# Kernel optimization log

Hardware: AMD Instinct MI355X
Metric: run time of the kernel (lower is better)

## Reference

```python
import jax, jax.numpy as jnp
import numpy as np
from jax.scipy.special import logsumexp

# Module hyperparameters
N_PARTS = 128
BATCH = 1024
# Entropic-regularized solver settings (differentiable surrogate for the
# cvxpylayers LP solve; eps small relative to O(1) eta-phi distances)
EPS = 0.02
ITERS = 100
LOG_FLOOR = 1e-30  # avoid log(0) for zero-mass dummy particles


def setup_inputs() -> dict:
    key = jax.random.key(0)
    k1, k2 = jax.random.split(key)
    # [B, n_parts, 3]: features (eta, phi, pt); uniform fill keeps pt > 0
    jets1 = jax.random.uniform(k1, (BATCH, N_PARTS, 3), dtype=jnp.float32)
    jets2 = jax.random.uniform(k2, (BATCH, N_PARTS, 3), dtype=jnp.float32)
    return {"jets1": jets1, "jets2": jets2}


def _sinkhorn_flow(C, loga, logb):
    """Batched log-domain Sinkhorn. C: [B,N,M], loga: [B,N], logb: [B,M].
    Returns the transport plan (flow) [B,N,M] with marginals ~ (a, b)."""
    f = jnp.zeros_like(loga)
    g = jnp.zeros_like(logb)

    def step(carry, _):
        f, g = carry
        f = EPS * (loga - logsumexp((g[:, None, :] - C) / EPS, axis=2))
        g = EPS * (logb - logsumexp((f[:, :, None] - C) / EPS, axis=1))
        return (f, g), None

    (f, g), _ = jax.lax.scan(step, (f, g), None, length=ITERS)
    return jnp.exp((f[:, :, None] + g[:, None, :] - C) / EPS)


def reference(jets1, jets2):
    n = jets1.shape[1]
    # Pairwise eta-phi ground distances: [B, n, n]
    diffs = -(jets1[:, :, None, :2] - jets2[:, None, :, :2]) + 1e-12
    dists = jnp.linalg.norm(diffs, axis=3)
    # pt weights (LP marginals)
    w1 = jets1[:, :, 2]
    w2 = jets2[:, :, 2]
    E1 = jnp.sum(w1, axis=1)
    E2 = jnp.sum(w2, axis=1)
    EabsDiff = jnp.abs(E2 - E1)
    # Partial OT (total mass = min(E1,E2), row/col sums <= w) is made balanced
    # by adding one zero-cost dummy particle per side absorbing the excess mass.
    a = jnp.concatenate([w1, jnp.maximum(E2 - E1, 0.0)[:, None]], axis=1)  # [B, n+1]
    b = jnp.concatenate([w2, jnp.maximum(E1 - E2, 0.0)[:, None]], axis=1)  # [B, n+1]
    Cp = jnp.pad(dists, ((0, 0), (0, 1), (0, 1)))  # dummy row/col have zero cost
    loga = jnp.log(jnp.maximum(a, LOG_FLOOR))
    logb = jnp.log(jnp.maximum(b, LOG_FLOOR))
    flow = _sinkhorn_flow(Cp, loga, logb)  # [B, n+1, n+1]
    # EMD = transport cost over real particles + energy-difference penalty
    emds = jnp.sum(dists * flow[:, :n, :n], axis=(1, 2)) + EabsDiff  # [B]
    return emds
```

## Files before the change

### kernel.cpp

```cpp
#include <hip/hip_runtime.h>

#define NP    128
#define NITER 100
#define RSC   72.13475204444817f
#define IRSC  0.013862943611198906f

typedef __attribute__((ext_vector_type(8))) short bf16x8;
typedef __attribute__((ext_vector_type(4))) float f32x4;

__device__ __forceinline__ float wsum64(float x) {
  #pragma unroll
  for (int s = 1; s < 64; s <<= 1) x += __shfl_xor(x, s);
  return x;
}
__device__ __forceinline__ float bf2f(unsigned short h) {
  return __uint_as_float(((unsigned)h) << 16);
}
__device__ __forceinline__ unsigned short f2bf(float f) {
  unsigned u = __float_as_uint(f);
  u += 0x7fffu + ((u >> 16) & 1u);
  return (unsigned short)(u >> 16);
}

__global__ __launch_bounds__(64, 1) void emd_sinkhorn(
    const float* __restrict__ j1g, const float* __restrict__ j2g,
    float* __restrict__ out)
{
  __shared__ __align__(16) float x1s[NP], y1s[NP], x2s[NP], y2s[NP];
  __shared__ __align__(16) float ahs[NP], bhs[NP];
  __shared__ __align__(16) float Slds[NP];
  __shared__ __align__(16) unsigned short Plds[NP];
  __shared__ __align__(16) unsigned short Qlds[NP];

  const int l  = threadIdx.x;
  const int lg = l >> 4;
  const int li = l & 15;
  const int b  = blockIdx.x;
  const float* J1 = j1g + (size_t)b * (NP * 3);
  const float* J2 = j2g + (size_t)b * (NP * 3);

  #pragma unroll
  for (int k = l; k < NP; k += 64) {
    x1s[k] = J1[3*k]; y1s[k] = J1[3*k+1]; ahs[k] = J1[3*k+2];
    x2s[k] = J2[3*k]; y2s[k] = J2[3*k+1]; bhs[k] = J2[3*k+2];
  }
  __syncthreads();

  const float e1 = wsum64(ahs[l] + ahs[l + 64]);
  const float e2 = wsum64(bhs[l] + bhs[l + 64]);
  const float dE = fabsf(e2 - e1);
  const float aslk = fmaxf(fmaxf(e2 - e1, 0.0f), 1e-30f);
  const float bslk = fmaxf(fmaxf(e1 - e2, 0.0f), 1e-30f);
  const float2 araw = *(const float2*)&ahs[2*l];
  const float2 braw = *(const float2*)&bhs[2*l];
  const float ah0 = fmaxf(araw.x, 1e-30f), ah1 = fmaxf(araw.y, 1e-30f);
  const float bh0 = fmaxf(braw.x, 1e-30f), bh1 = fmaxf(braw.y, 1e-30f);

  bf16x8 KA[8][4], KB[8][4];
  #pragma unroll
  for (int rt = 0; rt < 8; ++rt) {
    const float xr = x1s[16*rt + li], yr = y1s[16*rt + li];
    #pragma unroll
    for (int kt = 0; kt < 4; ++kt) {
      #pragma unroll
      for (int i2 = 0; i2 < 8; ++i2) {
        const int k = 32*kt + 8*lg + i2;
        const float dx = x2s[k] - xr + 1e-12f;
        const float dy = y2s[k] - yr + 1e-12f;
        KA[rt][kt][i2] = (short)f2bf(
            __builtin_amdgcn_exp2f(-__builtin_sqrtf(dx*dx + dy*dy) * RSC));
      }
    }
  }
  #pragma unroll
  for (int ct = 0; ct < 8; ++ct) {
    const float xc = x2s[16*ct + li], yc = y2s[16*ct + li];
    #pragma unroll
    for (int kt = 0; kt < 4; ++kt) {
      #pragma unroll
      for (int i2 = 0; i2 < 8; ++i2) {
        const int k = 32*kt + 8*lg + i2;
        const float dx = xc - x1s[k] + 1e-12f;
        const float dy = yc - y1s[k] + 1e-12f;
        KB[ct][kt][i2] = (short)f2bf(
            __builtin_amdgcn_exp2f(-__builtin_sqrtf(dx*dx + dy*dy) * RSC));
      }
    }
  }

  ((unsigned*)Qlds)[l] = 0x3F803F80u;
  float SQ = 128.0f, q128 = 1.0f;
  __syncthreads();

  for (int it = 0; it < NITER; ++it) {
    const float p128 = aslk * __builtin_amdgcn_rcpf(SQ + q128);

    bf16x8 qf[4];
    #pragma unroll
    for (int kt = 0; kt < 4; ++kt)
      qf[kt] = *(const bf16x8*)((const char*)Qlds + 64*kt + 16*lg);
    f32x4 acc[8];
    #pragma unroll
    for (int rt = 0; rt < 8; ++rt) {
      acc[rt] = (f32x4){q128, q128, q128, q128};
      #pragma unroll
      for (int kt = 0; kt < 4; ++kt)
        acc[rt] = __builtin_amdgcn_mfma_f32_16x16x32_bf16(
            KA[rt][kt], qf[kt], acc[rt], 0, 0, 0);
    }
    if (li == 0) {
      #pragma unroll
      for (int rt = 0; rt < 8; ++rt)
        *(f32x4*)&Slds[16*rt + 4*lg] = acc[rt];
    }
    __syncthreads();
    const float2 s2 = *(const float2*)&Slds[2*l];
    const float P0 = ah0 * __builtin_amdgcn_rcpf(s2.x);
    const float P1 = ah1 * __builtin_amdgcn_rcpf(s2.y);
    const float SP = wsum64(P0 + P1);
    const float q128n = bslk * __builtin_amdgcn_rcpf(SP + p128);
    ((unsigned*)Plds)[l] =
        (unsigned)f2bf(P0) | ((unsigned)f2bf(P1) << 16);
    __syncthreads();

    bf16x8 pf[4];
    #pragma unroll
    for (int kt = 0; kt < 4; ++kt)
      pf[kt] = *(const bf16x8*)((const char*)Plds + 64*kt + 16*lg);
    f32x4 acc2[8];
    #pragma unroll
    for (int ct = 0; ct < 8; ++ct) {
      acc2[ct] = (f32x4){p128, p128, p128, p128};
      #pragma unroll
      for (int kt = 0; kt < 4; ++kt)
        acc2[ct] = __builtin_amdgcn_mfma_f32_16x16x32_bf16(
            pf[kt], KB[ct][kt], acc2[ct], 0, 0, 0);
    }
    if (lg == 0) {
      #pragma unroll
      for (int ct = 0; ct < 8; ++ct)
        Slds[16*ct + li] = acc2[ct][0];
    }
    __syncthreads();
    const float2 t2 = *(const float2*)&Slds[2*l];
    const float Q0 = bh0 * __builtin_amdgcn_rcpf(t2.x);
    const float Q1 = bh1 * __builtin_amdgcn_rcpf(t2.y);
    SQ = wsum64(Q0 + Q1);
    ((unsigned*)Qlds)[l] =
        (unsigned)f2bf(Q0) | ((unsigned)f2bf(Q1) << 16);
    q128 = q128n;
    __syncthreads();
  }

  bf16x8 qf[4];
  #pragma unroll
  for (int kt = 0; kt < 4; ++kt)
    qf[kt] = *(const bf16x8*)((const char*)Qlds + 64*kt + 16*lg);
  float accE = 0.0f;
  #pragma unroll
  for (int rt = 0; rt < 8; ++rt) {
    const float Pn = bf2f(Plds[16*rt + li]);
    #pragma unroll
    for (int kt = 0; kt < 4; ++kt) {
      #pragma unroll
      for (int i2 = 0; i2 < 8; ++i2) {
        const float kk = bf2f((unsigned short)KA[rt][kt][i2]);
        const float qm = bf2f((unsigned short)qf[kt][i2]);
        const float d  = -__builtin_amdgcn_logf(kk) * IRSC;
        accE = fmaf(d, (Pn * kk) * qm, accE);
      }
    }
  }
  accE = wsum64(accE);
  if (l == 0) out[b] = accE + dE;
}

extern "C" void kernel_launch(void* const* d_in, const int* in_sizes, int n_in,
                              void* d_out, int out_size, void* d_ws, size_t ws_size,
                              hipStream_t stream) {
  const float* j1 = (const float*)d_in[0];
  const float* j2 = (const float*)d_in[1];
  float* outp = (float*)d_out;
  const int batch = in_sizes[0] / (NP * 3);
  hipLaunchKernelGGL(emd_sinkhorn, dim3(batch), dim3(64), 0, stream,
                     j1, j2, outp);
}
```

Measured before the change: 236.7 us.

## Split Sinkhorn matvecs across two waves and broadcast vectors via ds_bpermute

The block grows from one wave to two. Each wave holds half of the kernel matrices (4 row or column tiles instead of 8) and computes half of each matvec. Both waves redundantly compute the full P/Q vectors, and the MFMA operands are gathered from registers with ds_bpermute instead of LDS round trips. This drops two barriers per iteration, halves per-wave MFMA work and register footprint, and raises parallelism per batch element, at the cost of block-wide barriers between waves and duplicated scaling work.

Result: no change. 232.9 us (-1.6%).

```diff
diff --git a/kernel.cpp b/kernel.cpp
--- a/kernel.cpp
+++ b/kernel.cpp
@@ -22,27 +22,28 @@
   return (unsigned short)(u >> 16);
 }
 
-__global__ __launch_bounds__(64, 1) void emd_sinkhorn(
+__global__ __launch_bounds__(128, 2) void emd_sinkhorn(
     const float* __restrict__ j1g, const float* __restrict__ j2g,
     float* __restrict__ out)
 {
   __shared__ __align__(16) float x1s[NP], y1s[NP], x2s[NP], y2s[NP];
   __shared__ __align__(16) float ahs[NP], bhs[NP];
   __shared__ __align__(16) float Slds[NP];
-  __shared__ __align__(16) unsigned short Plds[NP];
-  __shared__ __align__(16) unsigned short Qlds[NP];
-
-  const int l  = threadIdx.x;
+  __shared__ __align__(16) float Tlds[NP];
+  __shared__ float red[2];
+
+  const int t  = threadIdx.x;
+  const int l  = t & 63;
+  const int wv = t >> 6;
   const int lg = l >> 4;
   const int li = l & 15;
   const int b  = blockIdx.x;
   const float* J1 = j1g + (size_t)b * (NP * 3);
   const float* J2 = j2g + (size_t)b * (NP * 3);
 
-  #pragma unroll
-  for (int k = l; k < NP; k += 64) {
-    x1s[k] = J1[3*k]; y1s[k] = J1[3*k+1]; ahs[k] = J1[3*k+2];
-    x2s[k] = J2[3*k]; y2s[k] = J2[3*k+1]; bhs[k] = J2[3*k+2];
+  if (t < NP) {
+    x1s[t] = J1[3*t]; y1s[t] = J1[3*t+1]; ahs[t] = J1[3*t+2];
+    x2s[t] = J2[3*t]; y2s[t] = J2[3*t+1]; bhs[t] = J2[3*t+2];
   }
   __syncthreads();
 
@@ -56,10 +57,11 @@
   const float ah0 = fmaxf(araw.x, 1e-30f), ah1 = fmaxf(araw.y, 1e-30f);
   const float bh0 = fmaxf(braw.x, 1e-30f), bh1 = fmaxf(braw.y, 1e-30f);
 
-  bf16x8 KA[8][4], KB[8][4];
-  #pragma unroll
-  for (int rt = 0; rt < 8; ++rt) {
-    const float xr = x1s[16*rt + li], yr = y1s[16*rt + li];
+  bf16x8 KA[4][4], KB[4][4];
+  #pragma unroll
+  for (int rt = 0; rt < 4; ++rt) {
+    const int n = 64*wv + 16*rt + li;
+    const float xr = x1s[n], yr = y1s[n];
     #pragma unroll
     for (int kt = 0; kt < 4; ++kt) {
       #pragma unroll
@@ -73,8 +75,9 @@
     }
   }
   #pragma unroll
-  for (int ct = 0; ct < 8; ++ct) {
-    const float xc = x2s[16*ct + li], yc = y2s[16*ct + li];
+  for (int ct = 0; ct < 4; ++ct) {
+    const int m = 64*wv + 16*ct + li;
+    const float xc = x2s[m], yc = y2s[m];
     #pragma unroll
     for (int kt = 0; kt < 4; ++kt) {
       #pragma unroll
@@ -88,20 +91,27 @@
     }
   }
 
-  ((unsigned*)Qlds)[l] = 0x3F803F80u;
+  unsigned Qpk = 0x3F803F80u;
+  unsigned Ppk = 0;
   float SQ = 128.0f, q128 = 1.0f;
-  __syncthreads();
 
   for (int it = 0; it < NITER; ++it) {
     const float p128 = aslk * __builtin_amdgcn_rcpf(SQ + q128);
 
     bf16x8 qf[4];
     #pragma unroll
-    for (int kt = 0; kt < 4; ++kt)
-      qf[kt] = *(const bf16x8*)((const char*)Qlds + 64*kt + 16*lg);
-    f32x4 acc[8];
-    #pragma unroll
-    for (int rt = 0; rt < 8; ++rt) {
+    for (int kt = 0; kt < 4; ++kt) {
+      union { unsigned u[4]; bf16x8 v; } r;
+      #pragma unroll
+      for (int q = 0; q < 4; ++q)
+        r.u[q] = (unsigned)__builtin_amdgcn_ds_bpermute(
+            4*(16*kt + 4*lg + q), (int)Qpk);
+      qf[kt] = r.v;
+    }
+
+    f32x4 acc[4];
+    #pragma unroll
+    for (int rt = 0; rt < 4; ++rt) {
       acc[rt] = (f32x4){q128, q128, q128, q128};
       #pragma unroll
       for (int kt = 0; kt < 4; ++kt)
@@ -110,26 +120,32 @@
     }
     if (li == 0) {
       #pragma unroll
-      for (int rt = 0; rt < 8; ++rt)
-        *(f32x4*)&Slds[16*rt + 4*lg] = acc[rt];
+      for (int rt = 0; rt < 4; ++rt)
+        *(f32x4*)&Slds[64*wv + 16*rt + 4*lg] = acc[rt];
     }
     __syncthreads();
+
     const float2 s2 = *(const float2*)&Slds[2*l];
     const float P0 = ah0 * __builtin_amdgcn_rcpf(s2.x);
     const float P1 = ah1 * __builtin_amdgcn_rcpf(s2.y);
     const float SP = wsum64(P0 + P1);
     const float q128n = bslk * __builtin_amdgcn_rcpf(SP + p128);
-    ((unsigned*)Plds)[l] =
-        (unsigned)f2bf(P0) | ((unsigned)f2bf(P1) << 16);
-    __syncthreads();
+    Ppk = (unsigned)f2bf(P0) | ((unsigned)f2bf(P1) << 16);
 
     bf16x8 pf[4];
     #pragma unroll
-    for (int kt = 0; kt < 4; ++kt)
-      pf[kt] = *(const bf16x8*)((const char*)Plds + 64*kt + 16*lg);
-    f32x4 acc2[8];
-    #pragma unroll
-    for (int ct = 0; ct < 8; ++ct) {
+    for (int kt = 0; kt < 4; ++kt) {
+      union { unsigned u[4]; bf16x8 v; } r;
+      #pragma unroll
+      for (int q = 0; q < 4; ++q)
+        r.u[q] = (unsigned)__builtin_amdgcn_ds_bpermute(
+            4*(16*kt + 4*lg + q), (int)Ppk);
+      pf[kt] = r.v;
+    }
+
+    f32x4 acc2[4];
+    #pragma unroll
+    for (int ct = 0; ct < 4; ++ct) {
       acc2[ct] = (f32x4){p128, p128, p128, p128};
       #pragma unroll
       for (int kt = 0; kt < 4; ++kt)
@@ -138,28 +154,36 @@
     }
     if (lg == 0) {
       #pragma unroll
-      for (int ct = 0; ct < 8; ++ct)
-        Slds[16*ct + li] = acc2[ct][0];
+      for (int ct = 0; ct < 4; ++ct)
+        Tlds[64*wv + 16*ct + li] = acc2[ct][0];
     }
     __syncthreads();
-    const float2 t2 = *(const float2*)&Slds[2*l];
+
+    const float2 t2 = *(const float2*)&Tlds[2*l];
     const float Q0 = bh0 * __builtin_amdgcn_rcpf(t2.x);
     const float Q1 = bh1 * __builtin_amdgcn_rcpf(t2.y);
     SQ = wsum64(Q0 + Q1);
-    ((unsigned*)Qlds)[l] =
-        (unsigned)f2bf(Q0) | ((unsigned)f2bf(Q1) << 16);
+    Qpk = (unsigned)f2bf(Q0) | ((unsigned)f2bf(Q1) << 16);
     q128 = q128n;
-    __syncthreads();
   }
 
   bf16x8 qf[4];
   #pragma unroll
-  for (int kt = 0; kt < 4; ++kt)
-    qf[kt] = *(const bf16x8*)((const char*)Qlds + 64*kt + 16*lg);
+  for (int kt = 0; kt < 4; ++kt) {
+    union { unsigned u[4]; bf16x8 v; } r;
+    #pragma unroll
+    for (int q = 0; q < 4; ++q)
+      r.u[q] = (unsigned)__builtin_amdgcn_ds_bpermute(
+          4*(16*kt + 4*lg + q), (int)Qpk);
+    qf[kt] = r.v;
+  }
   float accE = 0.0f;
   #pragma unroll
-  for (int rt = 0; rt < 8; ++rt) {
-    const float Pn = bf2f(Plds[16*rt + li]);
+  for (int rt = 0; rt < 4; ++rt) {
+    const int n = 64*wv + 16*rt + li;
+    const unsigned pr = (unsigned)__builtin_amdgcn_ds_bpermute(
+        4*(n >> 1), (int)Ppk);
+    const float Pn = bf2f((unsigned short)((li & 1) ? (pr >> 16) : pr));
     #pragma unroll
     for (int kt = 0; kt < 4; ++kt) {
       #pragma unroll
@@ -172,7 +196,9 @@
     }
   }
   accE = wsum64(accE);
-  if (l == 0) out[b] = accE + dE;
+  if (l == 0) red[wv] = accE;
+  __syncthreads();
+  if (t == 0) out[b] = (red[0] + red[1]) + dE;
 }
 
 extern "C" void kernel_launch(void* const* d_in, const int* in_sizes, int n_in,
@@ -182,6 +208,6 @@
   const float* j2 = (const float*)d_in[1];
   float* outp = (float*)d_out;
   const int batch = in_sizes[0] / (NP * 3);
-  hipLaunchKernelGGL(emd_sinkhorn, dim3(batch), dim3(64), 0, stream,
+  hipLaunchKernelGGL(emd_sinkhorn, dim3(batch), dim3(128), 0, stream,
                      j1, j2, outp);
 }
```

## Split each Sinkhorn problem across four wavefronts and drop redundant barriers

Applied to the files above, without the earlier changes.

Each block now uses 256 threads (four waves) instead of one wave. Each wave keeps a 32-row slice of the kernel matrices, so register use per wave drops and the serial MFMA chain per iteration is four times shorter. Every wave recomputes the full P and Q vectors and writes identical values to shared memory, which lets two of the four barriers per iteration go; a separate T buffer keeps the two matrix-vector phases from clobbering each other. The cost is redundant normalization work in every wave and a small cross-wave reduction at the end.

New measurement: 201.6 us. 1.17x faster.

```diff
diff --git a/kernel.cpp b/kernel.cpp
--- a/kernel.cpp
+++ b/kernel.cpp
@@ -22,27 +22,30 @@
   return (unsigned short)(u >> 16);
 }
 
-__global__ __launch_bounds__(64, 1) void emd_sinkhorn(
+__global__ __launch_bounds__(256, 2) void emd_sinkhorn(
     const float* __restrict__ j1g, const float* __restrict__ j2g,
     float* __restrict__ out)
 {
   __shared__ __align__(16) float x1s[NP], y1s[NP], x2s[NP], y2s[NP];
   __shared__ __align__(16) float ahs[NP], bhs[NP];
   __shared__ __align__(16) float Slds[NP];
+  __shared__ __align__(16) float Tlds[NP];
   __shared__ __align__(16) unsigned short Plds[NP];
   __shared__ __align__(16) unsigned short Qlds[NP];
+  __shared__ float red[4];
 
-  const int l  = threadIdx.x;
+  const int t  = threadIdx.x;
+  const int l  = t & 63;
+  const int wv = t >> 6;
   const int lg = l >> 4;
   const int li = l & 15;
   const int b  = blockIdx.x;
   const float* J1 = j1g + (size_t)b * (NP * 3);
   const float* J2 = j2g + (size_t)b * (NP * 3);
 
-  #pragma unroll
-  for (int k = l; k < NP; k += 64) {
-    x1s[k] = J1[3*k]; y1s[k] = J1[3*k+1]; ahs[k] = J1[3*k+2];
-    x2s[k] = J2[3*k]; y2s[k] = J2[3*k+1]; bhs[k] = J2[3*k+2];
+  if (t < NP) {
+    x1s[t] = J1[3*t]; y1s[t] = J1[3*t+1]; ahs[t] = J1[3*t+2];
+    x2s[t] = J2[3*t]; y2s[t] = J2[3*t+1]; bhs[t] = J2[3*t+2];
   }
   __syncthreads();
 
@@ -56,10 +59,11 @@
   const float ah0 = fmaxf(araw.x, 1e-30f), ah1 = fmaxf(araw.y, 1e-30f);
   const float bh0 = fmaxf(braw.x, 1e-30f), bh1 = fmaxf(braw.y, 1e-30f);
 
-  bf16x8 KA[8][4], KB[8][4];
+  bf16x8 KA[2][4], KB[2][4];
   #pragma unroll
-  for (int rt = 0; rt < 8; ++rt) {
-    const float xr = x1s[16*rt + li], yr = y1s[16*rt + li];
+  for (int rt = 0; rt < 2; ++rt) {
+    const int n = 32*wv + 16*rt + li;
+    const float xr = x1s[n], yr = y1s[n];
     #pragma unroll
     for (int kt = 0; kt < 4; ++kt) {
       #pragma unroll
@@ -73,8 +77,9 @@
     }
   }
   #pragma unroll
-  for (int ct = 0; ct < 8; ++ct) {
-    const float xc = x2s[16*ct + li], yc = y2s[16*ct + li];
+  for (int ct = 0; ct < 2; ++ct) {
+    const int m = 32*wv + 16*ct + li;
+    const float xc = x2s[m], yc = y2s[m];
     #pragma unroll
     for (int kt = 0; kt < 4; ++kt) {
       #pragma unroll
@@ -99,9 +104,9 @@
     #pragma unroll
     for (int kt = 0; kt < 4; ++kt)
       qf[kt] = *(const bf16x8*)((const char*)Qlds + 64*kt + 16*lg);
-    f32x4 acc[8];
+    f32x4 acc[2];
     #pragma unroll
-    for (int rt = 0; rt < 8; ++rt) {
+    for (int rt = 0; rt < 2; ++rt) {
       acc[rt] = (f32x4){q128, q128, q128, q128};
       #pragma unroll
       for (int kt = 0; kt < 4; ++kt)
@@ -110,26 +115,25 @@
     }
     if (li == 0) {
       #pragma unroll
-      for (int rt = 0; rt < 8; ++rt)
-        *(f32x4*)&Slds[16*rt + 4*lg] = acc[rt];
+      for (int rt = 0; rt < 2; ++rt)
+        *(f32x4*)&Slds[32*wv + 16*rt + 4*lg] = acc[rt];
     }
     __syncthreads();
+
     const float2 s2 = *(const float2*)&Slds[2*l];
     const float P0 = ah0 * __builtin_amdgcn_rcpf(s2.x);
     const float P1 = ah1 * __builtin_amdgcn_rcpf(s2.y);
     const float SP = wsum64(P0 + P1);
     const float q128n = bslk * __builtin_amdgcn_rcpf(SP + p128);
-    ((unsigned*)Plds)[l] =
-        (unsigned)f2bf(P0) | ((unsigned)f2bf(P1) << 16);
-    __syncthreads();
+    ((unsigned*)Plds)[l] = (unsigned)f2bf(P0) | ((unsigned)f2bf(P1) << 16);
 
     bf16x8 pf[4];
     #pragma unroll
     for (int kt = 0; kt < 4; ++kt)
       pf[kt] = *(const bf16x8*)((const char*)Plds + 64*kt + 16*lg);
-    f32x4 acc2[8];
+    f32x4 acc2[2];
     #pragma unroll
-    for (int ct = 0; ct < 8; ++ct) {
+    for (int ct = 0; ct < 2; ++ct) {
       acc2[ct] = (f32x4){p128, p128, p128, p128};
       #pragma unroll
       for (int kt = 0; kt < 4; ++kt)
@@ -138,18 +142,17 @@
     }
     if (lg == 0) {
       #pragma unroll
-      for (int ct = 0; ct < 8; ++ct)
-        Slds[16*ct + li] = acc2[ct][0];
+      for (int ct = 0; ct < 2; ++ct)
+        Tlds[32*wv + 16*ct + li] = acc2[ct][0];
     }
     __syncthreads();
-    const float2 t2 = *(const float2*)&Slds[2*l];
+
+    const float2 t2 = *(const float2*)&Tlds[2*l];
     const float Q0 = bh0 * __builtin_amdgcn_rcpf(t2.x);
     const float Q1 = bh1 * __builtin_amdgcn_rcpf(t2.y);
     SQ = wsum64(Q0 + Q1);
-    ((unsigned*)Qlds)[l] =
-        (unsigned)f2bf(Q0) | ((unsigned)f2bf(Q1) << 16);
+    ((unsigned*)Qlds)[l] = (unsigned)f2bf(Q0) | ((unsigned)f2bf(Q1) << 16);
     q128 = q128n;
-    __syncthreads();
   }
 
   bf16x8 qf[4];
@@ -158,8 +161,8 @@
     qf[kt] = *(const bf16x8*)((const char*)Qlds + 64*kt + 16*lg);
   float accE = 0.0f;
   #pragma unroll
-  for (int rt = 0; rt < 8; ++rt) {
-    const float Pn = bf2f(Plds[16*rt + li]);
+  for (int rt = 0; rt < 2; ++rt) {
+    const float Pn = bf2f(Plds[32*wv + 16*rt + li]);
     #pragma unroll
     for (int kt = 0; kt < 4; ++kt) {
       #pragma unroll
@@ -172,7 +175,9 @@
     }
   }
   accE = wsum64(accE);
-  if (l == 0) out[b] = accE + dE;
+  if (l == 0) red[wv] = accE;
+  __syncthreads();
+  if (t == 0) out[b] = ((red[0] + red[1]) + (red[2] + red[3])) + dE;
 }
 
 extern "C" void kernel_launch(void* const* d_in, const int* in_sizes, int n_in,
@@ -182,6 +187,6 @@
   const float* j2 = (const float*)d_in[1];
   float* outp = (float*)d_out;
   const int batch = in_sizes[0] / (NP * 3);
-  hipLaunchKernelGGL(emd_sinkhorn, dim3(batch), dim3(64), 0, stream,
+  hipLaunchKernelGGL(emd_sinkhorn, dim3(batch), dim3(256), 0, stream,
                      j1, j2, outp);
 }
```
